# Optimization experiments

Measured on AMD Instinct MI355X. Metric: run time of the kernel, lower is better.

Reference implementation:

```python
import jax, jax.numpy as jnp
import numpy as np

N_NODES = 100000
N_EDGES = 1600000
NUM_GRAPHS = 128


def setup_inputs() -> dict:
    key = jax.random.key(0)
    k1, k2, k3, k4, k5, k6 = jax.random.split(key, 6)
    x = jax.random.normal(k1, (N_NODES, 69), dtype=jnp.float32)
    src = jax.random.randint(k2, (N_EDGES,), 0, N_NODES)
    dst = jax.random.randint(k3, (N_EDGES,), 0, N_NODES)
    graph_ids = jnp.sort(jax.random.randint(k4, (N_NODES,), 0, NUM_GRAPHS))
    # Glorot-uniform weights like dgl GraphConv (bias=False)
    lim1 = np.sqrt(6.0 / (69 + 128))
    lim2 = np.sqrt(6.0 / (128 + 64))
    W1 = jax.random.uniform(k5, (69, 128), minval=-lim1, maxval=lim1, dtype=jnp.float32)
    W2 = jax.random.uniform(k6, (128, 64), minval=-lim2, maxval=lim2, dtype=jnp.float32)
    return {"x": x, "W1": W1, "W2": W2, "src": src, "dst": dst, "graph_ids": graph_ids}


def _graph_conv(feat, W, src, dst, inv_sqrt_out, inv_sqrt_in, n_nodes):
    # dgl GraphConv norm='both': D_out^{-1/2} -> SpMM(A) -> D_in^{-1/2} -> W
    h = feat * inv_sqrt_out[:, None]
    agg = jax.ops.segment_sum(h[src], dst, num_segments=n_nodes)  # [N, d]
    agg = agg * inv_sqrt_in[:, None]
    return agg @ W


def reference(x, W1, W2, src, dst, graph_ids):
    n = x.shape[0]
    ones = jnp.ones((src.shape[0],), dtype=x.dtype)
    out_deg = jax.ops.segment_sum(ones, src, num_segments=n)
    in_deg = jax.ops.segment_sum(ones, dst, num_segments=n)
    inv_sqrt_out = jax.lax.rsqrt(jnp.clip(out_deg, 1.0, None))
    inv_sqrt_in = jax.lax.rsqrt(jnp.clip(in_deg, 1.0, None))

    h = _graph_conv(x, W1, src, dst, inv_sqrt_out, inv_sqrt_in, n)
    h = jax.nn.relu(h)
    h = _graph_conv(h, W2, src, dst, inv_sqrt_out, inv_sqrt_in, n)
    h = jax.nn.relu(h)
    # dgl.max_nodes: per-graph max readout -> [num_graphs, 64]
    readout = jax.ops.segment_max(h, graph_ids, num_segments=NUM_GRAPHS)
    return readout
```

## Files before the change

kernel.cpp:

```cpp
#include <hip/hip_runtime.h>

#define N_NODES 100000
#define N_EDGES 1600000
#define NUM_GRAPHS 128

#define BSH 7
#define NBUCK 782
#define NBLKP 256
#define EPB (N_EDGES / NBLKP)
#define SOFF (NBUCK * NBLKP)
#define NSCAN (2 * NBUCK * NBLKP)
#define SCAN_BS 1024
#define NBSC ((NSCAN + SCAN_BS - 1) / SCAN_BS)

__global__ __launch_bounds__(256) void part_hist(const int* __restrict__ src,
                                                 const int* __restrict__ dst,
                                                 int* __restrict__ cnt) {
    __shared__ int hd[NBUCK], hs[NBUCK];
    for (int i = threadIdx.x; i < NBUCK; i += 256) { hd[i] = 0; hs[i] = 0; }
    __syncthreads();
    int bk = blockIdx.x;
    int e0 = bk * EPB;
    for (int j = threadIdx.x; j < EPB; j += 256) {
        int e = e0 + j;
        atomicAdd(&hd[dst[e] >> BSH], 1);
        atomicAdd(&hs[src[e] >> BSH], 1);
    }
    __syncthreads();
    for (int i = threadIdx.x; i < NBUCK; i += 256) {
        cnt[i * NBLKP + bk] = hd[i];
        cnt[SOFF + i * NBLKP + bk] = hs[i];
    }
}

__global__ __launch_bounds__(256) void scan1(const int* __restrict__ cnt, int* __restrict__ excl,
                                             int* __restrict__ blksum, int n) {
    __shared__ int tmp[256];
    int t = threadIdx.x;
    int idx0 = blockIdx.x * SCAN_BS + t * 4;
    int v[4];
#pragma unroll
    for (int k = 0; k < 4; ++k) { int i = idx0 + k; v[k] = (i < n) ? cnt[i] : 0; }
    int sum = v[0] + v[1] + v[2] + v[3];
    tmp[t] = sum;
    __syncthreads();
    for (int off = 1; off < 256; off <<= 1) {
        int y = (t >= off) ? tmp[t - off] : 0;
        __syncthreads();
        tmp[t] += y;
        __syncthreads();
    }
    int run = (t > 0) ? tmp[t - 1] : 0;
#pragma unroll
    for (int k = 0; k < 4; ++k) { int i = idx0 + k; if (i < n) excl[i] = run; run += v[k]; }
    if (t == 255) blksum[blockIdx.x] = tmp[255];
}

__global__ __launch_bounds__(256) void scan2(int* __restrict__ blksum, int nb) {
    __shared__ int tmp[256];
    int t = threadIdx.x;
    int v[4]; int s = 0;
#pragma unroll
    for (int k = 0; k < 4; ++k) { int i = t * 4 + k; v[k] = (i < nb) ? blksum[i] : 0; s += v[k]; }
    tmp[t] = s;
    __syncthreads();
    for (int off = 1; off < 256; off <<= 1) {
        int y = (t >= off) ? tmp[t - off] : 0;
        __syncthreads();
        tmp[t] += y;
        __syncthreads();
    }
    int run = (t > 0) ? tmp[t - 1] : 0;
#pragma unroll
    for (int k = 0; k < 4; ++k) { int i = t * 4 + k; if (i < nb) { int x = v[k]; blksum[i] = run; run += x; } }
}

__global__ void scan3(int* __restrict__ excl, const int* __restrict__ blkoff, int n) {
    int i = blockIdx.x * 256 + threadIdx.x;
    if (i < n) excl[i] += blkoff[i >> 10];
}

__global__ __launch_bounds__(256) void part_scatter(const int* __restrict__ src,
                                                    const int* __restrict__ dst,
                                                    const int* __restrict__ base,
                                                    unsigned* __restrict__ pdst,
                                                    unsigned char* __restrict__ psrc) {
    __shared__ int cd[NBUCK], cs[NBUCK];
    int bk = blockIdx.x;
    for (int i = threadIdx.x; i < NBUCK; i += 256) {
        cd[i] = base[i * NBLKP + bk];
        cs[i] = base[SOFF + i * NBLKP + bk] - N_EDGES;
    }
    __syncthreads();
    int e0 = bk * EPB;
    for (int j = threadIdx.x; j < EPB; j += 256) {
        int e = e0 + j;
        int s = src[e], d = dst[e];
        int pd = atomicAdd(&cd[d >> BSH], 1);
        pdst[pd] = (unsigned)s | ((unsigned)(d & 127) << 17);
        int ps = atomicAdd(&cs[s >> BSH], 1);
        psrc[ps] = (unsigned char)(s & 127);
    }
}

__global__ __launch_bounds__(256) void build_csr(const unsigned* __restrict__ pdst,
                                                 const int* __restrict__ base,
                                                 int* __restrict__ ecol, int* __restrict__ row_start,
                                                 float* __restrict__ isqi, int nN) {
    __shared__ int lh[128];
    __shared__ int lcur[128];
    int bu = blockIdx.x;
    int b0 = base[bu * NBLKP];
    int b1 = (bu == NBUCK - 1) ? N_EDGES : base[(bu + 1) * NBLKP];
    int t = threadIdx.x;
    if (t < 128) lh[t] = 0;
    __syncthreads();
    for (int j = b0 + t; j < b1; j += 256)
        atomicAdd(&lh[pdst[j] >> 17], 1);
    __syncthreads();
    int myc = (t < 128) ? lh[t] : 0;
    for (int off = 1; off < 128; off <<= 1) {
        int v = (t < 128 && t >= off) ? lh[t - off] : 0;
        __syncthreads();
        if (t < 128) lh[t] += v;
        __syncthreads();
    }
    if (t < 128) {
        int excl = lh[t] - myc;
        int node = (bu << BSH) + t;
        if (node < nN) {
            row_start[node] = b0 + excl;
            isqi[node] = rsqrtf(fmaxf((float)myc, 1.0f));
        }
        lcur[t] = b0 + excl;
    }
    __syncthreads();
    for (int j = b0 + t; j < b1; j += 256) {
        unsigned w = pdst[j];
        int off = w >> 17;
        int pos = atomicAdd(&lcur[off], 1);
        ecol[pos] = (int)(w & 0x1FFFFu);
    }
}

__global__ __launch_bounds__(256) void src_deg(const unsigned char* __restrict__ psrc,
                                               const int* __restrict__ base,
                                               float* __restrict__ isqo, int nN) {
    __shared__ int lh[128];
    int bu = blockIdx.x;
    int b0 = base[SOFF + bu * NBLKP] - N_EDGES;
    int b1 = (bu == NBUCK - 1) ? N_EDGES : base[SOFF + (bu + 1) * NBLKP] - N_EDGES;
    int t = threadIdx.x;
    if (t < 128) lh[t] = 0;
    __syncthreads();
    for (int j = b0 + t; j < b1; j += 256)
        atomicAdd(&lh[psrc[j]], 1);
    __syncthreads();
    if (t < 128) {
        int node = (bu << BSH) + t;
        if (node < nN) isqo[node] = rsqrtf(fmaxf((float)lh[t], 1.0f));
    }
}

__global__ void prescale_kernel(const float* __restrict__ x, const float* __restrict__ isqo,
                                float* __restrict__ xs, int nN) {
    int wave = (int)(((unsigned)blockIdx.x * blockDim.x + threadIdx.x) >> 6);
    int lane = threadIdx.x & 63;
    if (wave >= nN) return;
    float sc = isqo[wave];
    xs[(size_t)wave * 72 + lane] = x[(size_t)wave * 69 + lane] * sc;
    if (lane < 8)
        xs[(size_t)wave * 72 + 64 + lane] =
            (lane < 5) ? x[(size_t)wave * 69 + 64 + lane] * sc : 0.0f;
}

template<int D>
__global__ void gather_kernel(const float* __restrict__ feat, const int* __restrict__ ecol,
                              const int* __restrict__ row_start, const float* __restrict__ dscale,
                              float* __restrict__ agg, int nN, int nE) {
    int wave = (int)(((unsigned)blockIdx.x * blockDim.x + threadIdx.x) >> 6);
    int lane = threadIdx.x & 63;
    if (wave >= nN) return;
    int beg = row_start[wave];
    int end = (wave == nN - 1) ? nE : row_start[wave + 1];
    float acc0 = 0.0f, acc1 = 0.0f;
    for (int j0 = beg; j0 < end; j0 += 64) {
        int ne = min(64, end - j0);
        int eidx = (lane < ne) ? ecol[j0 + lane] : 0;
        int k = 0;
        for (; k + 4 <= ne; k += 4) {
            int s0 = __shfl(eidx, k),     s1 = __shfl(eidx, k + 1);
            int s2 = __shfl(eidx, k + 2), s3 = __shfl(eidx, k + 3);
            const float* f0 = feat + (size_t)s0 * D;
            const float* f1 = feat + (size_t)s1 * D;
            const float* f2 = feat + (size_t)s2 * D;
            const float* f3 = feat + (size_t)s3 * D;
            float a0 = f0[lane], a1 = f1[lane], a2 = f2[lane], a3 = f3[lane];
            if (D > 64 && lane < D - 64)
                acc1 += (f0[64 + lane] + f1[64 + lane]) + (f2[64 + lane] + f3[64 + lane]);
            acc0 += (a0 + a1) + (a2 + a3);
        }
        for (; k < ne; ++k) {
            int s = __shfl(eidx, k);
            const float* fr = feat + (size_t)s * D;
            acc0 += fr[lane];
            if (D > 64 && lane < D - 64) acc1 += fr[64 + lane];
        }
    }
    float dsc = dscale[wave];
    agg[(size_t)wave * D + lane] = acc0 * dsc;
    if (D > 64 && lane < D - 64) agg[(size_t)wave * D + 64 + lane] = acc1 * dsc;
}

template<int KP, int K, int NO, bool RELU, bool SCALE>
__global__ __launch_bounds__(256) void node_gemm(const float* __restrict__ in,
                                                 const float* __restrict__ W,
                                                 const float* __restrict__ rowscale,
                                                 float* __restrict__ out, int nN) {
    constexpr int CG = NO / 8;
    constexpr int RT = 256 / CG;
    constexpr int ROWS = RT * 4;
    __shared__ float Wl[KP * NO];
    for (int i = threadIdx.x; i < KP * NO; i += 256)
        Wl[i] = (i < K * NO) ? W[i] : 0.0f;
    __syncthreads();

    int cg = threadIdx.x % CG;
    int rt = threadIdx.x / CG;
    int row0 = blockIdx.x * ROWS + rt * 4;
    int c0 = cg * 8;

    float4 accL[4] = {};
    float4 accH[4] = {};
    int rclamp[4];
#pragma unroll
    for (int r = 0; r < 4; ++r) rclamp[r] = min(row0 + r, nN - 1);

#pragma unroll 2
    for (int k4 = 0; k4 < KP / 4; ++k4) {
        float4 a[4];
#pragma unroll
        for (int r = 0; r < 4; ++r)
            a[r] = *(const float4*)(in + (size_t)rclamp[r] * KP + k4 * 4);
#pragma unroll
        for (int kk = 0; kk < 4; ++kk) {
            int k = k4 * 4 + kk;
            float4 wlo = *(const float4*)&Wl[k * NO + c0];
            float4 whi = *(const float4*)&Wl[k * NO + c0 + 4];
#pragma unroll
            for (int r = 0; r < 4; ++r) {
                float ar = (kk == 0) ? a[r].x : (kk == 1) ? a[r].y : (kk == 2) ? a[r].z : a[r].w;
                accL[r].x += ar * wlo.x; accL[r].y += ar * wlo.y;
                accL[r].z += ar * wlo.z; accL[r].w += ar * wlo.w;
                accH[r].x += ar * whi.x; accH[r].y += ar * whi.y;
                accH[r].z += ar * whi.z; accH[r].w += ar * whi.w;
            }
        }
    }

#pragma unroll
    for (int r = 0; r < 4; ++r) {
        int row = row0 + r;
        if (row < nN) {
            float4 lo = accL[r], hi = accH[r];
            if (SCALE) {
                float sc = rowscale[row];
                lo.x *= sc; lo.y *= sc; lo.z *= sc; lo.w *= sc;
                hi.x *= sc; hi.y *= sc; hi.z *= sc; hi.w *= sc;
            }
            if (RELU) {
                lo.x = fmaxf(lo.x, 0.f); lo.y = fmaxf(lo.y, 0.f);
                lo.z = fmaxf(lo.z, 0.f); lo.w = fmaxf(lo.w, 0.f);
                hi.x = fmaxf(hi.x, 0.f); hi.y = fmaxf(hi.y, 0.f);
                hi.z = fmaxf(hi.z, 0.f); hi.w = fmaxf(hi.w, 0.f);
            }
            *(float4*)(out + (size_t)row * NO + c0) = lo;
            *(float4*)(out + (size_t)row * NO + c0 + 4) = hi;
        }
    }
}

__global__ void readout_kernel(const float* __restrict__ agg2, const int* __restrict__ gid,
                               unsigned* __restrict__ out, int nN) {
    const int NPW = 8;
    int wave = (int)(((unsigned)blockIdx.x * blockDim.x + threadIdx.x) >> 6);
    int lane = threadIdx.x & 63;
    int n0 = wave * NPW;
    if (n0 >= nN) return;
    int curg = gid[n0];
    float best = 0.0f;
    for (int i = 0; i < NPW; ++i) {
        int n = n0 + i;
        if (n >= nN) break;
        int g = gid[n];
        float v = fmaxf(agg2[(size_t)n * 64 + lane], 0.0f);
        if (g != curg) {
            atomicMax(&out[curg * 64 + lane], __float_as_uint(best));
            curg = g;
            best = v;
        } else {
            best = fmaxf(best, v);
        }
    }
    atomicMax(&out[curg * 64 + lane], __float_as_uint(best));
}

extern "C" void kernel_launch(void* const* d_in, const int* in_sizes, int n_in,
                              void* d_out, int out_size, void* d_ws, size_t ws_size,
                              hipStream_t stream) {
    const float* x   = (const float*)d_in[0];
    const float* W1  = (const float*)d_in[1];
    const float* W2  = (const float*)d_in[2];
    const int*   src = (const int*)d_in[3];
    const int*   dst = (const int*)d_in[4];
    const int*   gid = (const int*)d_in[5];

    char* w = (char*)d_ws;
    float* isqo    = (float*)w;                 w += N_NODES * 4;
    float* isqi    = (float*)w;                 w += N_NODES * 4;
    int* row_start = (int*)w;                   w += N_NODES * 4;
    int* ecol      = (int*)w;                   w += (size_t)N_EDGES * 4;
    int* cnt       = (int*)w;                   w += (size_t)NSCAN * 4;
    int* blksum    = (int*)w;                   w += 1024 * 4;
    float* bufA    = (float*)w;                 w += (size_t)N_NODES * 72 * 4;
    float* bufB    = (float*)w;
    unsigned* pdst      = (unsigned*)bufB;
    unsigned char* psrc = (unsigned char*)(bufB) + (size_t)N_EDGES * 4;
    float* xs = bufB;

    hipMemsetAsync(d_out, 0, (size_t)out_size * sizeof(float), stream);

    part_hist<<<NBLKP, 256, 0, stream>>>(src, dst, cnt);
    scan1<<<NBSC, 256, 0, stream>>>(cnt, cnt, blksum, NSCAN);
    scan2<<<1, 256, 0, stream>>>(blksum, NBSC);
    scan3<<<(NSCAN + 255) / 256, 256, 0, stream>>>(cnt, blksum, NSCAN);
    part_scatter<<<NBLKP, 256, 0, stream>>>(src, dst, cnt, pdst, psrc);
    build_csr<<<NBUCK, 256, 0, stream>>>(pdst, cnt, ecol, row_start, isqi, N_NODES);
    src_deg<<<NBUCK, 256, 0, stream>>>(psrc, cnt, isqo, N_NODES);

    prescale_kernel<<<(N_NODES * 64 + 255) / 256, 256, 0, stream>>>(x, isqo, xs, N_NODES);
    gather_kernel<72><<<(N_NODES * 64 + 255) / 256, 256, 0, stream>>>(
        xs, ecol, row_start, isqi, bufA, N_NODES, N_EDGES);
    node_gemm<72, 69, 128, true, false><<<(N_NODES + 63) / 64, 256, 0, stream>>>(
        bufA, W1, nullptr, bufB, N_NODES);

    node_gemm<128, 128, 64, false, true><<<(N_NODES + 127) / 128, 256, 0, stream>>>(
        bufB, W2, isqo, bufA, N_NODES);
    gather_kernel<64><<<(N_NODES * 64 + 255) / 256, 256, 0, stream>>>(
        bufA, ecol, row_start, isqi, bufB, N_NODES, N_EDGES);

    readout_kernel<<<((N_NODES + 7) / 8 * 64 + 255) / 256, 256, 0, stream>>>(
        bufB, gid, (unsigned*)d_out, N_NODES);
}
```

Measured before the change: 324.4 us.

## Vectorize gather with float2 loads, fuse prescale into src_deg, more partition blocks

The gather kernel now has each lane load a float2 and unrolls up to 16 edges, so more independent loads are in flight and fewer lanes sit idle on the second-half columns. The prescale of x is fused into the source-degree kernel, removing one launch and one read of isqo. The partition block count rises to 1000 for more parallelism, with scan2 generalized to handle the extra block sums. psrc is moved so it no longer aliases xs, because both are now live in the same kernel.

```diff
diff --git a/kernel.cpp b/kernel.cpp
--- a/kernel.cpp
+++ b/kernel.cpp
@@ -6,7 +6,7 @@
 
 #define BSH 7
 #define NBUCK 782
-#define NBLKP 256
+#define NBLKP 1000
 #define EPB (N_EDGES / NBLKP)
 #define SOFF (NBUCK * NBLKP)
 #define NSCAN (2 * NBUCK * NBLKP)
@@ -59,9 +59,10 @@
 __global__ __launch_bounds__(256) void scan2(int* __restrict__ blksum, int nb) {
     __shared__ int tmp[256];
     int t = threadIdx.x;
-    int v[4]; int s = 0;
-#pragma unroll
-    for (int k = 0; k < 4; ++k) { int i = t * 4 + k; v[k] = (i < nb) ? blksum[i] : 0; s += v[k]; }
+    int C = (nb + 255) / 256;
+    int base = t * C;
+    int s = 0;
+    for (int k = 0; k < C; ++k) { int i = base + k; if (i < nb) s += blksum[i]; }
     tmp[t] = s;
     __syncthreads();
     for (int off = 1; off < 256; off <<= 1) {
@@ -71,8 +72,10 @@
         __syncthreads();
     }
     int run = (t > 0) ? tmp[t - 1] : 0;
-#pragma unroll
-    for (int k = 0; k < 4; ++k) { int i = t * 4 + k; if (i < nb) { int x = v[k]; blksum[i] = run; run += x; } }
+    for (int k = 0; k < C; ++k) {
+        int i = base + k;
+        if (i < nb) { int v = blksum[i]; blksum[i] = run; run += v; }
+    }
 }
 
 __global__ void scan3(int* __restrict__ excl, const int* __restrict__ blkoff, int n) {
@@ -143,10 +146,13 @@
     }
 }
 
-__global__ __launch_bounds__(256) void src_deg(const unsigned char* __restrict__ psrc,
-                                               const int* __restrict__ base,
-                                               float* __restrict__ isqo, int nN) {
+__global__ __launch_bounds__(256) void src_deg_prescale(const unsigned char* __restrict__ psrc,
+                                                        const int* __restrict__ base,
+                                                        const float* __restrict__ x,
+                                                        float* __restrict__ isqo,
+                                                        float* __restrict__ xs, int nN) {
     __shared__ int lh[128];
+    __shared__ float sc[128];
     int bu = blockIdx.x;
     int b0 = base[SOFF + bu * NBLKP] - N_EDGES;
     int b1 = (bu == NBUCK - 1) ? N_EDGES : base[SOFF + (bu + 1) * NBLKP] - N_EDGES;
@@ -157,59 +163,79 @@
         atomicAdd(&lh[psrc[j]], 1);
     __syncthreads();
     if (t < 128) {
+        float v = rsqrtf(fmaxf((float)lh[t], 1.0f));
+        sc[t] = v;
         int node = (bu << BSH) + t;
-        if (node < nN) isqo[node] = rsqrtf(fmaxf((float)lh[t], 1.0f));
-    }
-}
-
-__global__ void prescale_kernel(const float* __restrict__ x, const float* __restrict__ isqo,
-                                float* __restrict__ xs, int nN) {
-    int wave = (int)(((unsigned)blockIdx.x * blockDim.x + threadIdx.x) >> 6);
-    int lane = threadIdx.x & 63;
-    if (wave >= nN) return;
-    float sc = isqo[wave];
-    xs[(size_t)wave * 72 + lane] = x[(size_t)wave * 69 + lane] * sc;
-    if (lane < 8)
-        xs[(size_t)wave * 72 + 64 + lane] =
-            (lane < 5) ? x[(size_t)wave * 69 + 64 + lane] * sc : 0.0f;
+        if (node < nN) isqo[node] = v;
+    }
+    __syncthreads();
+    int n0 = bu << BSH;
+    int rows = min(128, nN - n0);
+    for (int idx = t; idx < rows * 72; idx += 256) {
+        int r = idx / 72, c = idx - r * 72;
+        float val = (c < 69) ? x[(size_t)(n0 + r) * 69 + c] * sc[r] : 0.0f;
+        xs[(size_t)(n0 + r) * 72 + c] = val;
+    }
 }
 
 template<int D>
 __global__ void gather_kernel(const float* __restrict__ feat, const int* __restrict__ ecol,
                               const int* __restrict__ row_start, const float* __restrict__ dscale,
                               float* __restrict__ agg, int nN, int nE) {
+    constexpr int L = D / 2;
     int wave = (int)(((unsigned)blockIdx.x * blockDim.x + threadIdx.x) >> 6);
     int lane = threadIdx.x & 63;
     if (wave >= nN) return;
     int beg = row_start[wave];
     int end = (wave == nN - 1) ? nE : row_start[wave + 1];
-    float acc0 = 0.0f, acc1 = 0.0f;
+    float ax = 0.0f, ay = 0.0f;
+    bool act = (lane < L);
     for (int j0 = beg; j0 < end; j0 += 64) {
         int ne = min(64, end - j0);
         int eidx = (lane < ne) ? ecol[j0 + lane] : 0;
         int k = 0;
-        for (; k + 4 <= ne; k += 4) {
-            int s0 = __shfl(eidx, k),     s1 = __shfl(eidx, k + 1);
-            int s2 = __shfl(eidx, k + 2), s3 = __shfl(eidx, k + 3);
-            const float* f0 = feat + (size_t)s0 * D;
-            const float* f1 = feat + (size_t)s1 * D;
-            const float* f2 = feat + (size_t)s2 * D;
-            const float* f3 = feat + (size_t)s3 * D;
-            float a0 = f0[lane], a1 = f1[lane], a2 = f2[lane], a3 = f3[lane];
-            if (D > 64 && lane < D - 64)
-                acc1 += (f0[64 + lane] + f1[64 + lane]) + (f2[64 + lane] + f3[64 + lane]);
-            acc0 += (a0 + a1) + (a2 + a3);
+        for (; k + 16 <= ne; k += 16) {
+            float2 v[16];
+#pragma unroll
+            for (int u = 0; u < 16; ++u) {
+                int s = __shfl(eidx, k + u);
+                v[u] = act ? ((const float2*)(feat + (size_t)s * D))[lane] : make_float2(0.f, 0.f);
+            }
+#pragma unroll
+            for (int u = 0; u < 16; ++u) { ax += v[u].x; ay += v[u].y; }
+        }
+        if (k + 8 <= ne) {
+            float2 v[8];
+#pragma unroll
+            for (int u = 0; u < 8; ++u) {
+                int s = __shfl(eidx, k + u);
+                v[u] = act ? ((const float2*)(feat + (size_t)s * D))[lane] : make_float2(0.f, 0.f);
+            }
+#pragma unroll
+            for (int u = 0; u < 8; ++u) { ax += v[u].x; ay += v[u].y; }
+            k += 8;
+        }
+        if (k + 4 <= ne) {
+            float2 v[4];
+#pragma unroll
+            for (int u = 0; u < 4; ++u) {
+                int s = __shfl(eidx, k + u);
+                v[u] = act ? ((const float2*)(feat + (size_t)s * D))[lane] : make_float2(0.f, 0.f);
+            }
+#pragma unroll
+            for (int u = 0; u < 4; ++u) { ax += v[u].x; ay += v[u].y; }
+            k += 4;
         }
         for (; k < ne; ++k) {
             int s = __shfl(eidx, k);
-            const float* fr = feat + (size_t)s * D;
-            acc0 += fr[lane];
-            if (D > 64 && lane < D - 64) acc1 += fr[64 + lane];
-        }
-    }
-    float dsc = dscale[wave];
-    agg[(size_t)wave * D + lane] = acc0 * dsc;
-    if (D > 64 && lane < D - 64) agg[(size_t)wave * D + 64 + lane] = acc1 * dsc;
+            float2 v = act ? ((const float2*)(feat + (size_t)s * D))[lane] : make_float2(0.f, 0.f);
+            ax += v.x; ay += v.y;
+        }
+    }
+    if (act) {
+        float dsc = dscale[wave];
+        ((float2*)(agg + (size_t)wave * D))[lane] = make_float2(ax * dsc, ay * dsc);
+    }
 }
 
 template<int KP, int K, int NO, bool RELU, bool SCALE>
@@ -321,12 +347,12 @@
     int* row_start = (int*)w;                   w += N_NODES * 4;
     int* ecol      = (int*)w;                   w += (size_t)N_EDGES * 4;
     int* cnt       = (int*)w;                   w += (size_t)NSCAN * 4;
-    int* blksum    = (int*)w;                   w += 1024 * 4;
+    int* blksum    = (int*)w;                   w += 2048 * 4;
     float* bufA    = (float*)w;                 w += (size_t)N_NODES * 72 * 4;
     float* bufB    = (float*)w;
     unsigned* pdst      = (unsigned*)bufB;
-    unsigned char* psrc = (unsigned char*)(bufB) + (size_t)N_EDGES * 4;
-    float* xs = bufB;
+    float* xs           = bufB;
+    unsigned char* psrc = (unsigned char*)bufB + (size_t)N_NODES * 72 * 4;
 
     hipMemsetAsync(d_out, 0, (size_t)out_size * sizeof(float), stream);
 
@@ -336,9 +362,8 @@
     scan3<<<(NSCAN + 255) / 256, 256, 0, stream>>>(cnt, blksum, NSCAN);
     part_scatter<<<NBLKP, 256, 0, stream>>>(src, dst, cnt, pdst, psrc);
     build_csr<<<NBUCK, 256, 0, stream>>>(pdst, cnt, ecol, row_start, isqi, N_NODES);
-    src_deg<<<NBUCK, 256, 0, stream>>>(psrc, cnt, isqo, N_NODES);
-
-    prescale_kernel<<<(N_NODES * 64 + 255) / 256, 256, 0, stream>>>(x, isqo, xs, N_NODES);
+    src_deg_prescale<<<NBUCK, 256, 0, stream>>>(psrc, cnt, x, isqo, xs, N_NODES);
+
     gather_kernel<72><<<(N_NODES * 64 + 255) / 256, 256, 0, stream>>>(
         xs, ecol, row_start, isqi, bufA, N_NODES, N_EDGES);
     node_gemm<72, 69, 128, true, false><<<(N_NODES + 63) / 64, 256, 0, stream>>>(
```

New measurement: 345.4 us. 6.5% more time.
